# Kernel optimization log

Measured on AMD Instinct MI355X. Metric: run time of the kernel, lower is better.

## Reference

```python
import jax, jax.numpy as jnp
import numpy as np

N = 100000      # nodes
R = 4           # relations
E = 500000      # edges per relation
IN, HID, OUT = 256, 128, 64


def _graphconv(x, src, dst, W, b, n_nodes):
    """DGL GraphConv, norm='both': D_dst^{-1/2} A (D_src^{-1/2} x) W + b.
    Transform-first (in_feats >= out_feats path); math identical either way."""
    e = src.shape[0]
    ones = jnp.ones((e,), x.dtype)
    deg_out = jnp.clip(jax.ops.segment_sum(ones, src, num_segments=n_nodes), 1.0)
    deg_in = jnp.clip(jax.ops.segment_sum(ones, dst, num_segments=n_nodes), 1.0)
    h = (x * jax.lax.rsqrt(deg_out)[:, None]) @ W           # [N, out]
    agg = jax.ops.segment_sum(h[src], dst, num_segments=n_nodes)  # scatter-add over edges
    return agg * jax.lax.rsqrt(deg_in)[:, None] + b


def _hetero_layer(x, edges_src, edges_dst, W, b, n_nodes):
    # HeteroGraphConv(aggregate='sum'): sum of per-relation GraphConv outputs
    out = _graphconv(x, edges_src[0], edges_dst[0], W[0], b[0], n_nodes)
    for r in range(1, W.shape[0]):
        out = out + _graphconv(x, edges_src[r], edges_dst[r], W[r], b[r], n_nodes)
    return out


def setup_inputs() -> dict:
    key = jax.random.key(0)
    ks = jax.random.split(key, 8)
    x = jax.random.normal(ks[0], (N, IN), dtype=jnp.float32)
    edges_src = jax.random.randint(ks[1], (R, E), 0, N, dtype=jnp.int32)
    edges_dst = jax.random.randint(ks[2], (R, E), 0, N, dtype=jnp.int32)
    s1 = 1.0 / np.sqrt(IN)
    s2 = 1.0 / np.sqrt(HID)
    W1 = jax.random.uniform(ks[3], (R, IN, HID), jnp.float32, -s1, s1)
    b1 = jnp.zeros((R, HID), jnp.float32)
    W2 = jax.random.uniform(ks[4], (R, HID, OUT), jnp.float32, -s2, s2)
    b2 = jnp.zeros((R, OUT), jnp.float32)
    return {"x": x, "edges_src": edges_src, "edges_dst": edges_dst,
            "W1": W1, "b1": b1, "W2": W2, "b2": b2}


def reference(x, edges_src, edges_dst, W1, b1, W2, b2):
    h = _hetero_layer(x, edges_src, edges_dst, W1, b1, N)
    h = jax.nn.relu(h)
    out = _hetero_layer(h, edges_src, edges_dst, W2, b2, N)
    return out
```

## Files before the change

kernel.cpp:

```cpp
#include <hip/hip_runtime.h>

#define NN   100000
#define RR   4
#define EE   500000
#define FIN  256
#define FHID 128
#define FOUT 64
#define NBLK ((NN + 255) / 256)
#define NPAD (NN + 32)

#define PEDGE  ((RR * EE + 255) / 256)
#define PCW1   (RR * FIN * FHID / 256)
#define PCW2   (RR * FHID * FOUT / 256)
#define CONVW_GRID (PCW1 + PCW2 + 1)

#define NG1    ((NN + 127) / 128 * 4)
#define K1_PER 1564
#define K1_GRID (7 * K1_PER)

typedef unsigned short u16;
typedef unsigned char  u8;
typedef unsigned int   u32;
typedef __attribute__((ext_vector_type(8))) __bf16 bf16x8;
typedef __attribute__((ext_vector_type(4))) float  f32x4;
typedef __attribute__((ext_vector_type(4))) u32    u32x4;

__device__ __forceinline__ u16 f2bf(float f) {
    union { float f; u32 u; } v; v.f = f;
    u32 r = v.u + 0x7FFFu + ((v.u >> 16) & 1u);
    return (u16)(r >> 16);
}
__device__ __forceinline__ u32 pack2bf(float x, float y) {
    return ((u32)f2bf(y) << 16) | (u32)f2bf(x);
}

__device__ __forceinline__ float2 bfx2(u32 v) {
    union { u32 u; float f; } a, b;
    a.u = v << 16; b.u = v & 0xFFFF0000u;
    return {a.f, b.f};
}

typedef __attribute__((address_space(3))) u32 lds_u32;
typedef __attribute__((address_space(1))) const u32 gl_u32;
__device__ __forceinline__ void gload16(const void* g, void* l) {
    __builtin_amdgcn_global_load_lds((gl_u32*)g, (lds_u32*)l, 16, 0, 0);
}

__global__ __launch_bounds__(256) void convw_kernel(
        const float* __restrict__ W1, u16* __restrict__ W1t,
        const float* __restrict__ W2, u16* __restrict__ W2t,
        const float* __restrict__ b1, const float* __restrict__ b2,
        float* __restrict__ sb1, float* __restrict__ sb2) {
    int bx = blockIdx.x, t = threadIdx.x;
    if (bx < PCW1) {
        int i = bx * 256 + t;
        int r = i / (FIN * FHID);
        int rem = i - r * FIN * FHID;
        int k = rem / FHID, n = rem - k * FHID;
        W1t[((size_t)r * FHID + n) * FIN + k] = f2bf(W1[i]);
    } else if (bx < PCW1 + PCW2) {
        int i = (bx - PCW1) * 256 + t;
        int r = i / (FHID * FOUT);
        int rem = i - r * FHID * FOUT;
        int k = rem / FOUT, n = rem - k * FOUT;
        W2t[((size_t)r * FOUT + n) * FHID + k] = f2bf(W2[i]);
    } else {
        if (t < FHID) {
            float v = 0.f;
            for (int r = 0; r < RR; ++r) v += b1[r * FHID + t];
            sb1[t] = v;
        } else if (t < FHID + FOUT) {
            int j = t - FHID;
            float v = 0.f;
            for (int r = 0; r < RR; ++r) v += b2[r * FOUT + j];
            sb2[j] = v;
        }
    }
}

__device__ __forceinline__ void gemm1_body(u16* As, u16* Bs,
                                           const float* __restrict__ X,
                                           const u16* __restrict__ Bt,
                                           u16* __restrict__ Y, int M,
                                           int m0, int n0) {
    int tid = threadIdx.x;
    int wave = tid >> 6, lane = tid & 63;
    int quad = lane >> 4, l15 = lane & 15;
    int wm = (wave >> 1) * 64, wn = (wave & 1) * 64;

    int arow = tid >> 1;
    int acol = (tid & 1) * 16;
    const float4* Ag = (const float4*)(X + (size_t)min(m0 + arow, M - 1) * FIN + acol);
    u32* Aw = (u32*)As + arow * 16 + (acol >> 1);

    int srow = tid >> 2;
    int scol = (tid & 3) * 8;
    const u16* Bg0 = Bt + (size_t)(n0 + srow) * FIN + scol;
    const u16* Bg1 = Bt + (size_t)(n0 + srow + 64) * FIN + scol;
    u16* Bs0 = Bs + tid * 8;
    u16* Bs1 = Bs + 2048 + tid * 8;

    const bf16x8* Ard = (const bf16x8*)(As + (wm + l15) * 32 + quad * 8);
    const bf16x8* Brd = (const bf16x8*)(Bs + (wn + l15) * 32 + quad * 8);

    f32x4 acc[4][4] = {};
    for (int k0 = 0; k0 < FIN; k0 += 32) {
        gload16(Bg0 + k0, Bs0);
        gload16(Bg1 + k0, Bs1);
        float4 f0 = Ag[(k0 >> 2) + 0], f1 = Ag[(k0 >> 2) + 1];
        float4 f2 = Ag[(k0 >> 2) + 2], f3 = Ag[(k0 >> 2) + 3];
        u32x4 w0 = {pack2bf(f0.x, f0.y), pack2bf(f0.z, f0.w),
                    pack2bf(f1.x, f1.y), pack2bf(f1.z, f1.w)};
        u32x4 w1 = {pack2bf(f2.x, f2.y), pack2bf(f2.z, f2.w),
                    pack2bf(f3.x, f3.y), pack2bf(f3.z, f3.w)};
        ((u32x4*)Aw)[0] = w0;
        ((u32x4*)Aw)[1] = w1;
        __syncthreads();
        bf16x8 af[4], bfr[4];
#pragma unroll
        for (int i = 0; i < 4; ++i) af[i]  = Ard[i * 64];
#pragma unroll
        for (int j = 0; j < 4; ++j) bfr[j] = Brd[j * 64];
#pragma unroll
        for (int i = 0; i < 4; ++i)
#pragma unroll
            for (int j = 0; j < 4; ++j)
                acc[i][j] = __builtin_amdgcn_mfma_f32_16x16x32_bf16(af[i], bfr[j], acc[i][j], 0, 0, 0);
        __syncthreads();
    }

#pragma unroll
    for (int i = 0; i < 4; ++i) {
#pragma unroll
        for (int r = 0; r < 4; ++r) {
            int row = m0 + wm + i * 16 + quad * 4 + r;
            if (row < M) {
#pragma unroll
                for (int j = 0; j < 4; ++j) {
                    int col = n0 + wn + j * 16 + l15;
                    Y[(size_t)row * (RR * FHID) + col] = f2bf(acc[i][j][r]);
                }
            }
        }
    }
}

__global__ __launch_bounds__(256) void count_gemm(
        const float* __restrict__ x, const u16* __restrict__ W1t,
        u16* __restrict__ Y,
        const int* __restrict__ esrc, const int* __restrict__ edst,
        u32* __restrict__ counto, u32* __restrict__ counti,
        u8* __restrict__ pos8) {
    __shared__ u16 As[128 * 32];
    __shared__ u16 Bs[128 * 32];
    int p = blockIdx.x / 7, q = blockIdx.x - p * 7;
    if (q < 2) {
        int gb = p * 2 + q;
        if (gb >= NG1) return;
        gemm1_body(As, Bs, x, W1t, Y, NN, (gb >> 2) * 128, (gb & 3) * 128);
    } else {
        int i = (p * 5 + (q - 2)) * 256 + threadIdx.x;
        if (i >= RR * EE) return;
        int r = i / EE;
        int s = esrc[i], d = edst[i];
        atomicAdd(&counto[s], 1u << (8 * r));
        u32 old = atomicAdd(&counti[d], 1u << (8 * r));
        pos8[i] = (u8)((old >> (8 * r)) & 255u);
    }
}

__global__ __launch_bounds__(256) void reduce_deg(const u32* __restrict__ counto,
                                                  const u32* __restrict__ counti,
                                                  f32x4* __restrict__ so,
                                                  f32x4* __restrict__ si,
                                                  u32x4* __restrict__ di4,
                                                  int* __restrict__ cnt,
                                                  int* __restrict__ bsum) {
    __shared__ int sh[256];
    int n = blockIdx.x * 256 + threadIdx.x;
    int c = 0;
    if (n < NN) {
        u32 o = counto[n], d = counti[n];
        u32x4 dd;
        f32x4 vo, vi;
#pragma unroll
        for (int k = 0; k < 4; ++k) {
            u32 ob = (o >> (8 * k)) & 255u;
            u32 db = (d >> (8 * k)) & 255u;
            dd[k] = db;
            vo[k] = rsqrtf((float)max(ob, 1u));
            vi[k] = rsqrtf((float)max(db, 1u));
            c += (int)db;
        }
        so[n] = vo; si[n] = vi; di4[n] = dd;
        cnt[n] = c;
    }
    sh[threadIdx.x] = c;
    __syncthreads();
    for (int d = 128; d > 0; d >>= 1) {
        if (threadIdx.x < d) sh[threadIdx.x] += sh[threadIdx.x + d];
        __syncthreads();
    }
    if (threadIdx.x == 0) bsum[blockIdx.x] = sh[0];
}

__global__ __launch_bounds__(512) void scanb_kernel(const int* __restrict__ bsum,
                                                    int* __restrict__ boff) {
    __shared__ int sh[512];
    int t = threadIdx.x;
    int v = (t < NBLK) ? bsum[t] : 0;
    sh[t] = v;
    __syncthreads();
    for (int d = 1; d < 512; d <<= 1) {
        int u = (t >= d) ? sh[t - d] : 0;
        __syncthreads();
        sh[t] += u;
        __syncthreads();
    }
    if (t < NBLK) boff[t] = sh[t] - v;
}

__global__ __launch_bounds__(256) void offsets_kernel(const int* __restrict__ cnt,
                                                      const int* __restrict__ boff,
                                                      const u32x4* __restrict__ di4,
                                                      int* __restrict__ off,
                                                      u32x4* __restrict__ off4) {
    __shared__ int sh[256];
    int i = blockIdx.x * 256 + threadIdx.x;
    int t = threadIdx.x;
    int v = (i < NN) ? cnt[i] : 0;
    sh[t] = v;
    __syncthreads();
    for (int d = 1; d < 256; d <<= 1) {
        int u = (t >= d) ? sh[t - d] : 0;
        __syncthreads();
        sh[t] += u;
        __syncthreads();
    }
    int ex = boff[blockIdx.x] + sh[t] - v;
    if (i < NN) {
        off[i] = ex;
        u32x4 d = di4[i];
        u32x4 c;
        c[0] = (u32)ex;
        c[1] = c[0] + d[0];
        c[2] = c[1] + d[1];
        c[3] = c[2] + d[2];
        off4[i] = c;
    }
    if (i == NN - 1) off[NN] = ex + v;
}

__global__ __launch_bounds__(256) void place_kernel(const int* __restrict__ esrc,
                                                    const int* __restrict__ edst,
                                                    const u32* __restrict__ off4,
                                                    const u8* __restrict__ pos8,
                                                    u32* __restrict__ meta) {
    int i = blockIdx.x * 256 + threadIdx.x;
    if (i >= RR * EE) return;
    int r = i / EE;
    meta[off4[edst[i] * 4 + r] + pos8[i]] = (u32)(esrc[i] * 4 + r);
}

template<int NW, int K, int LOG2F>
__global__ __launch_bounds__(256) void gemm_tile(const u16* __restrict__ A,
                                                 const u16* __restrict__ Bt,
                                                 const f32x4* __restrict__ so,
                                                 u16* __restrict__ Y, int M) {
    __shared__ u16 As[128 * 32];
    __shared__ u16 Bs[128 * 32];
    int tid = threadIdx.x;
    int m0 = blockIdx.x * 128, n0 = blockIdx.y * 128;
    int wave = tid >> 6, lane = tid & 63;
    int quad = lane >> 4, l15 = lane & 15;
    int wm = (wave >> 1) * 64, wn = (wave & 1) * 64;

    int srow = tid >> 2;
    int scol = (tid & 3) * 8;
    const u16* Ag0 = A + (size_t)min(m0 + srow,      M - 1) * K + scol;
    const u16* Ag1 = A + (size_t)min(m0 + srow + 64, M - 1) * K + scol;
    const u16* Bg0 = Bt + (size_t)(n0 + srow) * K + scol;
    const u16* Bg1 = Bt + (size_t)(n0 + srow + 64) * K + scol;
    u16* As0 = As + tid * 8;
    u16* As1 = As + 2048 + tid * 8;
    u16* Bs0 = Bs + tid * 8;
    u16* Bs1 = Bs + 2048 + tid * 8;

    const bf16x8* Ard = (const bf16x8*)(As + (wm + l15) * 32 + quad * 8);
    const bf16x8* Brd = (const bf16x8*)(Bs + (wn + l15) * 32 + quad * 8);

    f32x4 acc[4][4] = {};
    for (int k0 = 0; k0 < K; k0 += 32) {
        gload16(Ag0 + k0, As0);
        gload16(Ag1 + k0, As1);
        gload16(Bg0 + k0, Bs0);
        gload16(Bg1 + k0, Bs1);
        __syncthreads();
        bf16x8 af[4], bfr[4];
#pragma unroll
        for (int i = 0; i < 4; ++i) af[i]  = Ard[i * 64];
#pragma unroll
        for (int j = 0; j < 4; ++j) bfr[j] = Brd[j * 64];
#pragma unroll
        for (int i = 0; i < 4; ++i)
#pragma unroll
            for (int j = 0; j < 4; ++j)
                acc[i][j] = __builtin_amdgcn_mfma_f32_16x16x32_bf16(af[i], bfr[j], acc[i][j], 0, 0, 0);
        __syncthreads();
    }

#pragma unroll
    for (int i = 0; i < 4; ++i) {
#pragma unroll
        for (int r = 0; r < 4; ++r) {
            int row = m0 + wm + i * 16 + quad * 4 + r;
            if (row < M) {
                f32x4 so4 = so[row];
#pragma unroll
                for (int j = 0; j < 4; ++j) {
                    int colb = n0 + wn + j * 16;
                    float scale = so4[colb >> LOG2F];
                    Y[(size_t)row * NW + colb + l15] = f2bf(acc[i][j][r] * scale);
                }
            }
        }
    }
}


__global__ __launch_bounds__(256) void gather1(const u32* __restrict__ Y,
                                               const int* __restrict__ off,
                                               const u32* __restrict__ meta,
                                               const float* __restrict__ soF,
                                               const f32x4* __restrict__ si,
                                               const float* __restrict__ sb,
                                               u32* __restrict__ H1) {
    int wid  = blockIdx.x * 4 + (threadIdx.x >> 6);
    int lane = threadIdx.x & 63;
    if (wid >= NN) return;
    int j = off[wid], end = off[wid + 1];
    f32x4 si4 = si[wid];
    float a0x = 0.f, a0y = 0.f, a1x = 0.f, a1y = 0.f;
    float a2x = 0.f, a2y = 0.f, a3x = 0.f, a3y = 0.f;
    for (; j + 4 <= end; j += 4) {
        u32 m0 = meta[j], m1 = meta[j + 1], m2 = meta[j + 2], m3 = meta[j + 3];
        u32 v0 = Y[(size_t)m0 * 64 + lane];
        u32 v1 = Y[(size_t)m1 * 64 + lane];
        u32 v2 = Y[(size_t)m2 * 64 + lane];
        u32 v3 = Y[(size_t)m3 * 64 + lane];
        float c0 = soF[m0] * si4[m0 & 3], c1 = soF[m1] * si4[m1 & 3];
        float c2 = soF[m2] * si4[m2 & 3], c3 = soF[m3] * si4[m3 & 3];
        float2 f0 = bfx2(v0), f1 = bfx2(v1), f2 = bfx2(v2), f3 = bfx2(v3);
        a0x = fmaf(c0, f0.x, a0x); a0y = fmaf(c0, f0.y, a0y);
        a1x = fmaf(c1, f1.x, a1x); a1y = fmaf(c1, f1.y, a1y);
        a2x = fmaf(c2, f2.x, a2x); a2y = fmaf(c2, f2.y, a2y);
        a3x = fmaf(c3, f3.x, a3x); a3y = fmaf(c3, f3.y, a3y);
    }
    for (; j < end; ++j) {
        u32 m0 = meta[j];
        u32 v0 = Y[(size_t)m0 * 64 + lane];
        float2 f0 = bfx2(v0);
        float c0 = soF[m0] * si4[m0 & 3];
        a0x = fmaf(c0, f0.x, a0x); a0y = fmaf(c0, f0.y, a0y);
    }
    float2 b = ((const float2*)sb)[lane];
    float ax = fmaxf((a0x + a1x) + (a2x + a3x) + b.x, 0.f);
    float ay = fmaxf((a0y + a1y) + (a2y + a3y) + b.y, 0.f);
    H1[(size_t)wid * 64 + lane] = ((u32)f2bf(ay) << 16) | (u32)f2bf(ax);
}

__global__ __launch_bounds__(256) void gather2(const u32* __restrict__ Y,
                                               const int* __restrict__ off,
                                               const u32* __restrict__ meta,
                                               const f32x4* __restrict__ si,
                                               const float* __restrict__ sb,
                                               float* __restrict__ out) {
    int wid  = blockIdx.x * 4 + (threadIdx.x >> 6);
    int lane = threadIdx.x & 63;
    if (wid >= NN) return;
    int sub = lane >> 5, col = lane & 31;
    int end = off[wid + 1];
    int j = off[wid] + sub;
    f32x4 si4 = si[wid];
    float a0x = 0.f, a0y = 0.f, a1x = 0.f, a1y = 0.f;
    for (; j + 2 < end; j += 4) {
        u32 m0 = meta[j], m1 = meta[j + 2];
        u32 v0 = Y[(size_t)m0 * 32 + col];
        u32 v1 = Y[(size_t)m1 * 32 + col];
        float2 f0 = bfx2(v0), f1 = bfx2(v1);
        float c0 = si4[m0 & 3], c1 = si4[m1 & 3];
        a0x = fmaf(c0, f0.x, a0x); a0y = fmaf(c0, f0.y, a0y);
        a1x = fmaf(c1, f1.x, a1x); a1y = fmaf(c1, f1.y, a1y);
    }
    if (j < end) {
        u32 m0 = meta[j];
        u32 v0 = Y[(size_t)m0 * 32 + col];
        float2 f0 = bfx2(v0);
        float c0 = si4[m0 & 3];
        a0x = fmaf(c0, f0.x, a0x); a0y = fmaf(c0, f0.y, a0y);
    }
    float ax = a0x + a1x, ay = a0y + a1y;
    ax += __shfl_xor(ax, 32);
    ay += __shfl_xor(ay, 32);
    if (sub == 0) {
        float2 b = ((const float2*)sb)[col];
        float2 o = {ax + b.x, ay + b.y};
        ((float2*)out)[(size_t)wid * 32 + col] = o;
    }
}


extern "C" void kernel_launch(void* const* d_in, const int* in_sizes, int n_in,
                              void* d_out, int out_size, void* d_ws, size_t ws_size,
                              hipStream_t stream) {
    const float* x    = (const float*)d_in[0];
    const int*   esrc = (const int*)  d_in[1];
    const int*   edst = (const int*)  d_in[2];
    const float* W1   = (const float*)d_in[3];
    const float* b1   = (const float*)d_in[4];
    const float* W2   = (const float*)d_in[5];
    const float* b2   = (const float*)d_in[6];
    float* out = (float*)d_out;

    char* w = (char*)d_ws;
    auto alloc = [&](size_t bytes) -> char* {
        char* p = w; w += (bytes + 255) & ~(size_t)255; return p;
    };
    u32*   cnt2    = (u32*)  alloc((size_t)2 * NPAD * 4);
    u32*   counto  = cnt2;
    u32*   counti  = cnt2 + NPAD;
    float* so      = (float*)alloc((size_t)NN * 4 * 4);
    float* si      = (float*)alloc((size_t)NN * 4 * 4);
    u32*   di4     = (u32*)  alloc((size_t)NN * 4 * 4);
    int*   cnt     = (int*)  alloc((size_t)NN * 4);
    int*   off     = (int*)  alloc((size_t)(NN + 1) * 4);
    u32*   off4    = (u32*)  alloc((size_t)NN * 4 * 4);
    int*   bsum    = (int*)  alloc((size_t)NBLK * 4);
    int*   boff    = (int*)  alloc((size_t)NBLK * 4);
    float* sb1     = (float*)alloc(FHID * 4);
    float* sb2     = (float*)alloc(FOUT * 4);
    u8*    pos8    = (u8*)   alloc((size_t)RR * EE);
    u16*   W1t     = (u16*)  alloc((size_t)RR * FIN * FHID * 2);
    u16*   W2t     = (u16*)  alloc((size_t)RR * FHID * FOUT * 2);
    u32*   meta    = (u32*)  alloc((size_t)RR * EE * 4);
    u16*   H1bf    = (u16*)  alloc((size_t)NN * FHID * 2);
    u16*   Yall    = (u16*)  alloc((size_t)NN * RR * FHID * 2);

    hipMemsetAsync(cnt2, 0, (size_t)2 * NPAD * 4, stream);

    convw_kernel<<<CONVW_GRID, 256, 0, stream>>>(W1, W1t, W2, W2t, b1, b2, sb1, sb2);

    count_gemm<<<K1_GRID, 256, 0, stream>>>(x, W1t, Yall, esrc, edst,
                                            counto, counti, pos8);

    reduce_deg<<<NBLK, 256, 0, stream>>>(counto, counti,
                                         (f32x4*)so, (f32x4*)si, (u32x4*)di4, cnt, bsum);
    scanb_kernel<<<1, 512, 0, stream>>>(bsum, boff);
    offsets_kernel<<<NBLK, 256, 0, stream>>>(cnt, boff, (const u32x4*)di4, off, (u32x4*)off4);
    place_kernel<<<PEDGE, 256, 0, stream>>>(esrc, edst, off4, pos8, meta);

    gather1<<<(NN + 3) / 4, 256, 0, stream>>>((const u32*)Yall, off, meta,
                                              so, (const f32x4*)si, sb1, (u32*)H1bf);

    {
        dim3 grid((NN + 127) / 128, (RR * FOUT) / 128);
        gemm_tile<RR * FOUT, FHID, 6><<<grid, 256, 0, stream>>>(H1bf, W2t, (const f32x4*)so, Yall, NN);
    }
    gather2<<<(NN + 3) / 4, 256, 0, stream>>>((const u32*)Yall, off, meta,
                                              (const f32x4*)si, sb2, out);
}
```

Measured before the change: 551.4 us.

## Count source degrees with LDS-privatized range histograms and rebalance fused grid

```diff
diff --git a/kernel.cpp b/kernel.cpp
--- a/kernel.cpp
+++ b/kernel.cpp
@@ -14,9 +14,13 @@
 #define PCW2   (RR * FHID * FOUT / 256)
 #define CONVW_GRID (PCW1 + PCW2 + 1)
 
-#define NG1    ((NN + 127) / 128 * 4)
-#define K1_PER 1564
-#define K1_GRID (7 * K1_PER)
+#define NG1     ((NN + 127) / 128 * 4)
+#define K1_GRID (29 * 391)
+#define SRCR    17
+#define SRCS    23
+#define RSZ     5883
+#define SSTRIDE 100352
+#define SLICE   ((RR * EE + SRCS - 1) / SRCS)
 
 typedef unsigned short u16;
 typedef unsigned char  u8;
@@ -88,15 +92,14 @@
     int quad = lane >> 4, l15 = lane & 15;
     int wm = (wave >> 1) * 64, wn = (wave & 1) * 64;
 
-    int arow = tid >> 1;
-    int acol = (tid & 1) * 16;
-    const float4* Ag = (const float4*)(X + (size_t)min(m0 + arow, M - 1) * FIN + acol);
-    u32* Aw = (u32*)As + arow * 16 + (acol >> 1);
-
-    int srow = tid >> 2;
-    int scol = (tid & 3) * 8;
-    const u16* Bg0 = Bt + (size_t)(n0 + srow) * FIN + scol;
-    const u16* Bg1 = Bt + (size_t)(n0 + srow + 64) * FIN + scol;
+    int srow  = tid >> 2;
+    int scol8 = (tid & 3) * 8;
+    const float* Ag0 = X + (size_t)min(m0 + srow,      M - 1) * FIN + scol8;
+    const float* Ag1 = X + (size_t)min(m0 + srow + 64, M - 1) * FIN + scol8;
+    const u16* Bg0 = Bt + (size_t)(n0 + srow) * FIN + scol8;
+    const u16* Bg1 = Bt + (size_t)(n0 + srow + 64) * FIN + scol8;
+    u32* Aw0 = (u32*)As + tid * 4;
+    u32* Aw1 = (u32*)(As + 2048) + tid * 4;
     u16* Bs0 = Bs + tid * 8;
     u16* Bs1 = Bs + 2048 + tid * 8;
 
@@ -107,14 +110,16 @@
     for (int k0 = 0; k0 < FIN; k0 += 32) {
         gload16(Bg0 + k0, Bs0);
         gload16(Bg1 + k0, Bs1);
-        float4 f0 = Ag[(k0 >> 2) + 0], f1 = Ag[(k0 >> 2) + 1];
-        float4 f2 = Ag[(k0 >> 2) + 2], f3 = Ag[(k0 >> 2) + 3];
-        u32x4 w0 = {pack2bf(f0.x, f0.y), pack2bf(f0.z, f0.w),
-                    pack2bf(f1.x, f1.y), pack2bf(f1.z, f1.w)};
-        u32x4 w1 = {pack2bf(f2.x, f2.y), pack2bf(f2.z, f2.w),
-                    pack2bf(f3.x, f3.y), pack2bf(f3.z, f3.w)};
-        ((u32x4*)Aw)[0] = w0;
-        ((u32x4*)Aw)[1] = w1;
+        float4 a0 = *(const float4*)(Ag0 + k0);
+        float4 a1 = *(const float4*)(Ag0 + k0 + 4);
+        float4 a2 = *(const float4*)(Ag1 + k0);
+        float4 a3 = *(const float4*)(Ag1 + k0 + 4);
+        u32x4 w0 = {pack2bf(a0.x, a0.y), pack2bf(a0.z, a0.w),
+                    pack2bf(a1.x, a1.y), pack2bf(a1.z, a1.w)};
+        u32x4 w1 = {pack2bf(a2.x, a2.y), pack2bf(a2.z, a2.w),
+                    pack2bf(a3.x, a3.y), pack2bf(a3.z, a3.w)};
+        *(u32x4*)Aw0 = w0;
+        *(u32x4*)Aw1 = w1;
         __syncthreads();
         bf16x8 af[4], bfr[4];
 #pragma unroll
@@ -149,28 +154,42 @@
         const float* __restrict__ x, const u16* __restrict__ W1t,
         u16* __restrict__ Y,
         const int* __restrict__ esrc, const int* __restrict__ edst,
-        u32* __restrict__ counto, u32* __restrict__ counti,
-        u8* __restrict__ pos8) {
-    __shared__ u16 As[128 * 32];
-    __shared__ u16 Bs[128 * 32];
-    int p = blockIdx.x / 7, q = blockIdx.x - p * 7;
-    if (q < 2) {
-        int gb = p * 2 + q;
-        if (gb >= NG1) return;
+        u32* __restrict__ counti, u8* __restrict__ pos8,
+        u32* __restrict__ srcpart) {
+    __shared__ u32 smem[5888];
+    int p = blockIdx.x / 29, q = blockIdx.x - p * 29;
+    if (q < 8) {
+        int gb = p * 8 + q;
+        u16* As = (u16*)smem;
+        u16* Bs = As + 4096;
         gemm1_body(As, Bs, x, W1t, Y, NN, (gb >> 2) * 128, (gb & 3) * 128);
+    } else if (q < 28) {
+        int i = (p * 20 + (q - 8)) * 256 + threadIdx.x;
+        if (i >= RR * EE) return;
+        u32 r = (u32)i / EE;
+        u32 old = atomicAdd(&counti[edst[i]], 1u << (8 * r));
+        pos8[i] = (u8)((old >> (8 * r)) & 255u);
     } else {
-        int i = (p * 5 + (q - 2)) * 256 + threadIdx.x;
-        if (i >= RR * EE) return;
-        int r = i / EE;
-        int s = esrc[i], d = edst[i];
-        atomicAdd(&counto[s], 1u << (8 * r));
-        u32 old = atomicAdd(&counti[d], 1u << (8 * r));
-        pos8[i] = (u8)((old >> (8 * r)) & 255u);
-    }
-}
-
-__global__ __launch_bounds__(256) void reduce_deg(const u32* __restrict__ counto,
-                                                  const u32* __restrict__ counti,
+        int g = p / SRCS, s = p - g * SRCS;
+        int base = g * RSZ;
+        for (int j = threadIdx.x; j < RSZ; j += 256) smem[j] = 0;
+        __syncthreads();
+        int lo = s * SLICE, hi = min(RR * EE, lo + SLICE);
+        for (int i = lo + threadIdx.x; i < hi; i += 256) {
+            int sn = esrc[i] - base;
+            if ((u32)sn < (u32)RSZ) {
+                u32 r = (u32)i / EE;
+                atomicAdd(&smem[sn], 1u << (8 * r));
+            }
+        }
+        __syncthreads();
+        u32* dst = srcpart + (size_t)s * SSTRIDE + base;
+        for (int j = threadIdx.x; j < RSZ; j += 256) dst[j] = smem[j];
+    }
+}
+
+__global__ __launch_bounds__(256) void reduce_deg(const u32* __restrict__ counti,
+                                                  const u32* __restrict__ srcpart,
                                                   f32x4* __restrict__ so,
                                                   f32x4* __restrict__ si,
                                                   u32x4* __restrict__ di4,
@@ -180,7 +199,10 @@
     int n = blockIdx.x * 256 + threadIdx.x;
     int c = 0;
     if (n < NN) {
-        u32 o = counto[n], d = counti[n];
+        u32 o = 0;
+#pragma unroll
+        for (int s = 0; s < SRCS; ++s) o += srcpart[(size_t)s * SSTRIDE + n];
+        u32 d = counti[n];
         u32x4 dd;
         f32x4 vo, vi;
 #pragma unroll
@@ -426,9 +448,8 @@
     auto alloc = [&](size_t bytes) -> char* {
         char* p = w; w += (bytes + 255) & ~(size_t)255; return p;
     };
-    u32*   cnt2    = (u32*)  alloc((size_t)2 * NPAD * 4);
-    u32*   counto  = cnt2;
-    u32*   counti  = cnt2 + NPAD;
+    u32*   counti  = (u32*)  alloc((size_t)NPAD * 4);
+    u32*   srcpart = (u32*)  alloc((size_t)SRCS * SSTRIDE * 4);
     float* so      = (float*)alloc((size_t)NN * 4 * 4);
     float* si      = (float*)alloc((size_t)NN * 4 * 4);
     u32*   di4     = (u32*)  alloc((size_t)NN * 4 * 4);
@@ -446,14 +467,14 @@
     u16*   H1bf    = (u16*)  alloc((size_t)NN * FHID * 2);
     u16*   Yall    = (u16*)  alloc((size_t)NN * RR * FHID * 2);
 
-    hipMemsetAsync(cnt2, 0, (size_t)2 * NPAD * 4, stream);
+    hipMemsetAsync(counti, 0, (size_t)NPAD * 4, stream);
 
     convw_kernel<<<CONVW_GRID, 256, 0, stream>>>(W1, W1t, W2, W2t, b1, b2, sb1, sb2);
 
     count_gemm<<<K1_GRID, 256, 0, stream>>>(x, W1t, Yall, esrc, edst,
-                                            counto, counti, pos8);
-
-    reduce_deg<<<NBLK, 256, 0, stream>>>(counto, counti,
+                                            counti, pos8, srcpart);
+
+    reduce_deg<<<NBLK, 256, 0, stream>>>(counti, srcpart,
                                          (f32x4*)so, (f32x4*)si, (u32x4*)di4, cnt, bsum);
     scanb_kernel<<<1, 512, 0, stream>>>(bsum, boff);
     offsets_kernel<<<NBLK, 256, 0, stream>>>(cnt, boff, (const u32x4*)di4, off, (u32x4*)off4);
```

Measured after the change: 655.6 us. 18.9% more time.
